# Kernel tuning notes

Measured on AMD Instinct MI355X. Metric: run time of the kernel, lower is better.

## Reference

```python
import jax, jax.numpy as jnp
import numpy as np

N = 131072
MUL = 128                      # multiplicity of each irrep block in the input
IN_DIM = MUL * (1 + 3 + 5)     # 128x0e + 128x1o + 128x2e = 1152
INV_SQRT_MUL = 1.0 / np.sqrt(MUL)  # e3nn o3.Linear path normalization (fan_in = 128)

# --- Clebsch-Gordan (wigner 3j) tensors for 1o x 1o -> 0e, 1e, 2e ------------
# e3nn real basis ordering for l=1 is (y, z, x): index 0=y, 1=z, 2=x.

def _w3j_110():
    # 0e output: dot product; sum of squares of entries = 1
    return np.eye(3, dtype=np.float32) / np.sqrt(3.0)

def _w3j_111():
    # 1e output: Levi-Civita (cross product), normalized so sum of squares = 1
    eps = np.zeros((3, 3, 3), np.float32)
    for i, j, k in [(0, 1, 2), (1, 2, 0), (2, 0, 1)]:
        eps[i, j, k] = 1.0
        eps[j, i, k] = -1.0
    return eps / np.sqrt(6.0)

def _w3j_112():
    # 2e output: symmetric traceless rank-2 part.
    # l=2 component order: (xy, yz, 3z^2-r^2, xz, x^2-y^2); l=1 axes (y,z,x).
    Y, Z, X = 0, 1, 2
    s2 = 1.0 / np.sqrt(2.0)
    s6 = 1.0 / np.sqrt(6.0)
    M = np.zeros((3, 3, 5), np.float32)
    M[X, Y, 0] = M[Y, X, 0] = s2
    M[Y, Z, 1] = M[Z, Y, 1] = s2
    M[X, X, 2] = -s6; M[Y, Y, 2] = -s6; M[Z, Z, 2] = 2.0 * s6
    M[X, Z, 3] = M[Z, X, 3] = s2
    M[X, X, 4] = s2; M[Y, Y, 4] = -s2
    return M / np.sqrt(5.0)

_C0 = jnp.asarray(_w3j_110())
_C1 = jnp.asarray(_w3j_111())
_C2 = jnp.asarray(_w3j_112())
# path weights sqrt(dim(irrep_out)) for irrep_normalization='component',
# path_normalization='element' with fan = mul1*mul2 = 1
_PW0 = 1.0
_PW1 = float(np.sqrt(3.0))
_PW2 = float(np.sqrt(5.0))


def setup_inputs() -> dict:
    key = jax.random.key(0)
    k1, k2, k3, k4 = jax.random.split(key, 4)
    x = jax.random.normal(k1, (N, IN_DIM), jnp.float32)
    W1 = jax.random.normal(k2, (MUL, MUL), jnp.float32)   # 128x1o -> 128x1o
    W2 = jax.random.normal(k3, (MUL, 2), jnp.float32)     # 128x1o -> 2x1o
    tp_w = jax.random.normal(k4, (3,), jnp.float32)       # one weight per CG path
    return {"x": x, "W1": W1, "W2": W2, "tp_w": tp_w}


def reference(x, W1, W2, tp_w):
    n = x.shape[0]
    # o3.Linear(128x0e+128x1o+128x2e -> 128x1o): only the 1o block connects.
    x1o = x[:, MUL:MUL + 3 * MUL].reshape(n, MUL, 3)
    y = jnp.einsum('nuc,uv->nvc', x1o, W1) * INV_SQRT_MUL   # [N,128,3]
    y = jax.nn.silu(y)                                      # elementwise, as in torch
    y = jnp.einsum('nuc,uv->nvc', y, W2) * INV_SQRT_MUL     # [N,2,3] == 2x1o
    a, b = y[:, 0], y[:, 1]                                 # split y[:, :3], y[:, 3:]
    out0 = (tp_w[0] * _PW0) * jnp.einsum('ij,ni,nj->n', _C0, a, b)[:, None]  # [N,1]
    out1 = (tp_w[1] * _PW1) * jnp.einsum('ijk,ni,nj->nk', _C1, a, b)          # [N,3]
    out2 = (tp_w[2] * _PW2) * jnp.einsum('ijk,ni,nj->nk', _C2, a, b)          # [N,5]
    return jnp.concatenate([out0, out1, out2], axis=-1)     # [N,9] (0e+1e+2e)
```

## Files before the change

kernel.cpp:

```cpp
#include <hip/hip_runtime.h>
#include <hip/hip_bf16.h>

#define MULC 128
#define IN_DIM 1152
#define ROWS_PER_WG 64
#define NTHREADS 256

typedef __attribute__((ext_vector_type(8))) short bf16x8;
typedef __attribute__((ext_vector_type(4))) float f32x4;
typedef __attribute__((ext_vector_type(4))) unsigned short u16x4;

#define W1T_PITCH 136
#define A_BASE 17408
#define A_PITCH 40
#define A_PLANE 2560

__device__ __forceinline__ unsigned short f2bf(float f) {
    unsigned int b = __builtin_bit_cast(unsigned int, f);
    b += 0x7fffu + ((b >> 16) & 1u);
    return (unsigned short)(b >> 16);
}

__global__ __launch_bounds__(NTHREADS, 2)
void nltp_kernel(const float* __restrict__ x, const float* __restrict__ W1,
                 const float* __restrict__ W2, const float* __restrict__ tpw,
                 float* __restrict__ out)
{
    __shared__ __align__(16) unsigned short lds[25088];
    const int t  = threadIdx.x;
    const int n0 = blockIdx.x * ROWS_PER_WG;
    const int l  = t & 63;
    const int w  = t >> 6;
    const int g  = l >> 4;
    const int li = l & 15;

    for (int it = 0; it < 16; ++it) {
        int tau = it * 256 + t;
        int v   = tau & 127;
        int u   = (tau >> 7) * 4;
        float f0 = W1[(u + 0) * MULC + v];
        float f1 = W1[(u + 1) * MULC + v];
        float f2 = W1[(u + 2) * MULC + v];
        float f3 = W1[(u + 3) * MULC + v];
        u16x4 pk = { f2bf(f0), f2bf(f1), f2bf(f2), f2bf(f3) };
        *(u16x4*)&lds[v * W1T_PITCH + u] = pk;
    }

    f32x4 acc[3][8];
#pragma unroll
    for (int c = 0; c < 3; ++c)
#pragma unroll
        for (int nt = 0; nt < 8; ++nt)
            acc[c][nt] = (f32x4){0.f, 0.f, 0.f, 0.f};

    for (int kc = 0; kc < 4; ++kc) {
        __syncthreads();
#pragma unroll
        for (int q = 0; q < 2; ++q) {
            int idx = q * 256 + t;
            int r   = idx >> 3;
            int j   = idx & 7;
            const float* src = x + (size_t)(n0 + r) * IN_DIM + MULC + kc * 96 + j * 12;
            float4 v0 = *(const float4*)(src);
            float4 v1 = *(const float4*)(src + 4);
            float4 v2 = *(const float4*)(src + 8);
            u16x4 p0 = { f2bf(v0.x), f2bf(v0.w), f2bf(v1.z), f2bf(v2.y) };
            u16x4 p1 = { f2bf(v0.y), f2bf(v1.x), f2bf(v1.w), f2bf(v2.z) };
            u16x4 p2 = { f2bf(v0.z), f2bf(v1.y), f2bf(v2.x), f2bf(v2.w) };
            int base = A_BASE + r * A_PITCH + 4 * j;
            *(u16x4*)&lds[base]              = p0;
            *(u16x4*)&lds[base + A_PLANE]    = p1;
            *(u16x4*)&lds[base + 2 * A_PLANE] = p2;
        }
        __syncthreads();

        bf16x8 af[3];
#pragma unroll
        for (int c = 0; c < 3; ++c)
            af[c] = *(const bf16x8*)&lds[A_BASE + c * A_PLANE + (16 * w + li) * A_PITCH + g * 8];
#pragma unroll
        for (int nt = 0; nt < 8; ++nt) {
            bf16x8 bf = *(const bf16x8*)&lds[(nt * 16 + li) * W1T_PITCH + kc * 32 + g * 8];
#pragma unroll
            for (int c = 0; c < 3; ++c)
                acc[c][nt] = __builtin_amdgcn_mfma_f32_16x16x32_bf16(af[c], bf, acc[c][nt], 0, 0, 0);
        }
    }

    const float inv = 0.08838834764831845f;
    float w2a[8], w2b[8];
#pragma unroll
    for (int nt = 0; nt < 8; ++nt) {
        float2 p = *(const float2*)(W2 + 2 * (nt * 16 + li));
        w2a[nt] = p.x; w2b[nt] = p.y;
    }
    float pa[3][4], pb[3][4];
#pragma unroll
    for (int c = 0; c < 3; ++c)
#pragma unroll
        for (int rg = 0; rg < 4; ++rg) { pa[c][rg] = 0.f; pb[c][rg] = 0.f; }

#pragma unroll
    for (int c = 0; c < 3; ++c)
#pragma unroll
        for (int nt = 0; nt < 8; ++nt)
#pragma unroll
            for (int rg = 0; rg < 4; ++rg) {
                float y = acc[c][nt][rg] * inv;
                float s = y / (1.f + __expf(-y));
                pa[c][rg] += s * w2a[nt];
                pb[c][rg] += s * w2b[nt];
            }

#pragma unroll
    for (int c = 0; c < 3; ++c)
#pragma unroll
        for (int rg = 0; rg < 4; ++rg) {
            float va = pa[c][rg], vb = pb[c][rg];
            va += __shfl_xor(va, 1, 16); vb += __shfl_xor(vb, 1, 16);
            va += __shfl_xor(va, 2, 16); vb += __shfl_xor(vb, 2, 16);
            va += __shfl_xor(va, 4, 16); vb += __shfl_xor(vb, 4, 16);
            va += __shfl_xor(va, 8, 16); vb += __shfl_xor(vb, 8, 16);
            pa[c][rg] = va * inv;
            pb[c][rg] = vb * inv;
        }

    const float tw0 = tpw[0], tw1 = tpw[1], tw2 = tpw[2];
    const float k0 = tw0 * 0.5773502691896258f;
    const float k1 = tw1 * 0.7071067811865476f;
    const float s2 = 0.7071067811865476f;
    const float s6 = 0.4082482904638631f;

#pragma unroll
    for (int rg = 0; rg < 4; ++rg) {
        float a0 = pa[0][rg], a1 = pa[1][rg], a2 = pa[2][rg];
        float b0 = pb[0][rg], b1 = pb[1][rg], b2 = pb[2][rg];
        float o0 = k0 * (a0 * b0 + a1 * b1 + a2 * b2);
        float o1 = k1 * (a1 * b2 - a2 * b1);
        float o2 = k1 * (a2 * b0 - a0 * b2);
        float o3 = k1 * (a0 * b1 - a1 * b0);
        float o4 = tw2 * (s2 * (a2 * b0 + a0 * b2));
        float o5 = tw2 * (s2 * (a0 * b1 + a1 * b0));
        float o6 = tw2 * (s6 * (2.f * a1 * b1 - a2 * b2 - a0 * b0));
        float o7 = tw2 * (s2 * (a2 * b1 + a1 * b2));
        float o8 = tw2 * (s2 * (a2 * b2 - a0 * b0));
        float o = li == 0 ? o0 : li == 1 ? o1 : li == 2 ? o2 : li == 3 ? o3 :
                  li == 4 ? o4 : li == 5 ? o5 : li == 6 ? o6 : li == 7 ? o7 : o8;
        if (li < 9) {
            int row = n0 + 16 * w + 4 * g + rg;
            out[row * 9 + li] = o;
        }
    }
}

extern "C" void kernel_launch(void* const* d_in, const int* in_sizes, int n_in,
                              void* d_out, int out_size, void* d_ws, size_t ws_size,
                              hipStream_t stream) {
    const float* x   = (const float*)d_in[0];
    const float* W1  = (const float*)d_in[1];
    const float* W2  = (const float*)d_in[2];
    const float* tpw = (const float*)d_in[3];
    float* out = (float*)d_out;
    const int n = in_sizes[0] / IN_DIM;
    dim3 grid(n / ROWS_PER_WG);
    nltp_kernel<<<grid, NTHREADS, 0, stream>>>(x, W1, W2, tpw, out);
}
```

Before: 62.81 us.

## Load x fragments directly into registers with double-buffered prefetch, drop LDS staging

Each lane now loads its own 24 contiguous floats of x per k-chunk straight into registers and converts them to bf16 MFMA A-fragments, instead of staging them through LDS with barriers. Loads for the next chunk are issued before the current chunk's MFMAs, and the first chunk load overlaps the W1 transpose into LDS. This removes per-chunk LDS writes, reads and syncthreads and shrinks LDS use. In exchange it raises register pressure, and the global loads are less coalesced across lanes.

```diff
diff --git a/kernel.cpp b/kernel.cpp
--- a/kernel.cpp
+++ b/kernel.cpp
@@ -5,15 +5,11 @@
 #define IN_DIM 1152
 #define ROWS_PER_WG 64
 #define NTHREADS 256
+#define W1T_PITCH 136
 
 typedef __attribute__((ext_vector_type(8))) short bf16x8;
 typedef __attribute__((ext_vector_type(4))) float f32x4;
 typedef __attribute__((ext_vector_type(4))) unsigned short u16x4;
-
-#define W1T_PITCH 136
-#define A_BASE 17408
-#define A_PITCH 40
-#define A_PLANE 2560
 
 __device__ __forceinline__ unsigned short f2bf(float f) {
     unsigned int b = __builtin_bit_cast(unsigned int, f);
@@ -21,18 +17,47 @@
     return (unsigned short)(b >> 16);
 }
 
+#define LOADC(r0,r1,r2,r3,r4,r5, kc) {                                  \
+    const float4* p_ = (const float4*)(xbase + 96 * (kc));              \
+    r0 = p_[0]; r1 = p_[1]; r2 = p_[2]; r3 = p_[3]; r4 = p_[4]; r5 = p_[5]; }
+
+#define FRAGS(F0,F1,F2, r0,r1,r2,r3,r4,r5)                                         \
+    bf16x8 F0 = { (short)f2bf(r0.x), (short)f2bf(r0.w), (short)f2bf(r1.z),         \
+                  (short)f2bf(r2.y), (short)f2bf(r3.x), (short)f2bf(r3.w),         \
+                  (short)f2bf(r4.z), (short)f2bf(r5.y) };                          \
+    bf16x8 F1 = { (short)f2bf(r0.y), (short)f2bf(r1.x), (short)f2bf(r1.w),         \
+                  (short)f2bf(r2.z), (short)f2bf(r3.y), (short)f2bf(r4.x),         \
+                  (short)f2bf(r4.w), (short)f2bf(r5.z) };                          \
+    bf16x8 F2 = { (short)f2bf(r0.z), (short)f2bf(r1.y), (short)f2bf(r2.x),         \
+                  (short)f2bf(r2.w), (short)f2bf(r3.z), (short)f2bf(r4.y),         \
+                  (short)f2bf(r5.x), (short)f2bf(r5.w) };
+
+#define MFMA_STEP(kc, F0,F1,F2)                                                     \
+    _Pragma("unroll")                                                               \
+    for (int nt = 0; nt < 8; ++nt) {                                                \
+        bf16x8 bfr = *(const bf16x8*)&lds[(nt * 16 + li) * W1T_PITCH + (kc) * 32 + g * 8]; \
+        acc[0][nt] = __builtin_amdgcn_mfma_f32_16x16x32_bf16(F0, bfr, acc[0][nt], 0, 0, 0); \
+        acc[1][nt] = __builtin_amdgcn_mfma_f32_16x16x32_bf16(F1, bfr, acc[1][nt], 0, 0, 0); \
+        acc[2][nt] = __builtin_amdgcn_mfma_f32_16x16x32_bf16(F2, bfr, acc[2][nt], 0, 0, 0); \
+    }
+
 __global__ __launch_bounds__(NTHREADS, 2)
 void nltp_kernel(const float* __restrict__ x, const float* __restrict__ W1,
                  const float* __restrict__ W2, const float* __restrict__ tpw,
                  float* __restrict__ out)
 {
-    __shared__ __align__(16) unsigned short lds[25088];
+    __shared__ __align__(16) unsigned short lds[128 * W1T_PITCH];
     const int t  = threadIdx.x;
     const int n0 = blockIdx.x * ROWS_PER_WG;
     const int l  = t & 63;
     const int w  = t >> 6;
     const int g  = l >> 4;
     const int li = l & 15;
+
+    const float* xbase = x + (size_t)(n0 + 16 * w + li) * IN_DIM + MULC + 24 * g;
+
+    float4 a0,a1,a2,a3,a4,a5, b0,b1,b2,b3,b4,b5;
+    LOADC(a0,a1,a2,a3,a4,a5, 0);
 
     for (int it = 0; it < 16; ++it) {
         int tau = it * 256 + t;
@@ -45,6 +70,7 @@
         u16x4 pk = { f2bf(f0), f2bf(f1), f2bf(f2), f2bf(f3) };
         *(u16x4*)&lds[v * W1T_PITCH + u] = pk;
     }
+    __syncthreads();
 
     f32x4 acc[3][8];
 #pragma unroll
@@ -53,39 +79,13 @@
         for (int nt = 0; nt < 8; ++nt)
             acc[c][nt] = (f32x4){0.f, 0.f, 0.f, 0.f};
 
-    for (int kc = 0; kc < 4; ++kc) {
-        __syncthreads();
-#pragma unroll
-        for (int q = 0; q < 2; ++q) {
-            int idx = q * 256 + t;
-            int r   = idx >> 3;
-            int j   = idx & 7;
-            const float* src = x + (size_t)(n0 + r) * IN_DIM + MULC + kc * 96 + j * 12;
-            float4 v0 = *(const float4*)(src);
-            float4 v1 = *(const float4*)(src + 4);
-            float4 v2 = *(const float4*)(src + 8);
-            u16x4 p0 = { f2bf(v0.x), f2bf(v0.w), f2bf(v1.z), f2bf(v2.y) };
-            u16x4 p1 = { f2bf(v0.y), f2bf(v1.x), f2bf(v1.w), f2bf(v2.z) };
-            u16x4 p2 = { f2bf(v0.z), f2bf(v1.y), f2bf(v2.x), f2bf(v2.w) };
-            int base = A_BASE + r * A_PITCH + 4 * j;
-            *(u16x4*)&lds[base]              = p0;
-            *(u16x4*)&lds[base + A_PLANE]    = p1;
-            *(u16x4*)&lds[base + 2 * A_PLANE] = p2;
-        }
-        __syncthreads();
-
-        bf16x8 af[3];
-#pragma unroll
-        for (int c = 0; c < 3; ++c)
-            af[c] = *(const bf16x8*)&lds[A_BASE + c * A_PLANE + (16 * w + li) * A_PITCH + g * 8];
-#pragma unroll
-        for (int nt = 0; nt < 8; ++nt) {
-            bf16x8 bf = *(const bf16x8*)&lds[(nt * 16 + li) * W1T_PITCH + kc * 32 + g * 8];
-#pragma unroll
-            for (int c = 0; c < 3; ++c)
-                acc[c][nt] = __builtin_amdgcn_mfma_f32_16x16x32_bf16(af[c], bf, acc[c][nt], 0, 0, 0);
-        }
-    }
+    LOADC(b0,b1,b2,b3,b4,b5, 1);
+    { FRAGS(fa0,fa1,fa2, a0,a1,a2,a3,a4,a5); MFMA_STEP(0, fa0,fa1,fa2); }
+    LOADC(a0,a1,a2,a3,a4,a5, 2);
+    { FRAGS(fb0,fb1,fb2, b0,b1,b2,b3,b4,b5); MFMA_STEP(1, fb0,fb1,fb2); }
+    LOADC(b0,b1,b2,b3,b4,b5, 3);
+    { FRAGS(fc0,fc1,fc2, a0,a1,a2,a3,a4,a5); MFMA_STEP(2, fc0,fc1,fc2); }
+    { FRAGS(fd0,fd1,fd2, b0,b1,b2,b3,b4,b5); MFMA_STEP(3, fd0,fd1,fd2); }
 
     const float inv = 0.08838834764831845f;
     float w2a[8], w2b[8];
@@ -133,17 +133,17 @@
 
 #pragma unroll
     for (int rg = 0; rg < 4; ++rg) {
-        float a0 = pa[0][rg], a1 = pa[1][rg], a2 = pa[2][rg];
-        float b0 = pb[0][rg], b1 = pb[1][rg], b2 = pb[2][rg];
-        float o0 = k0 * (a0 * b0 + a1 * b1 + a2 * b2);
-        float o1 = k1 * (a1 * b2 - a2 * b1);
-        float o2 = k1 * (a2 * b0 - a0 * b2);
-        float o3 = k1 * (a0 * b1 - a1 * b0);
-        float o4 = tw2 * (s2 * (a2 * b0 + a0 * b2));
-        float o5 = tw2 * (s2 * (a0 * b1 + a1 * b0));
-        float o6 = tw2 * (s6 * (2.f * a1 * b1 - a2 * b2 - a0 * b0));
-        float o7 = tw2 * (s2 * (a2 * b1 + a1 * b2));
-        float o8 = tw2 * (s2 * (a2 * b2 - a0 * b0));
+        float a_0 = pa[0][rg], a_1 = pa[1][rg], a_2 = pa[2][rg];
+        float b_0 = pb[0][rg], b_1 = pb[1][rg], b_2 = pb[2][rg];
+        float o0 = k0 * (a_0 * b_0 + a_1 * b_1 + a_2 * b_2);
+        float o1 = k1 * (a_1 * b_2 - a_2 * b_1);
+        float o2 = k1 * (a_2 * b_0 - a_0 * b_2);
+        float o3 = k1 * (a_0 * b_1 - a_1 * b_0);
+        float o4 = tw2 * (s2 * (a_2 * b_0 + a_0 * b_2));
+        float o5 = tw2 * (s2 * (a_0 * b_1 + a_1 * b_0));
+        float o6 = tw2 * (s6 * (2.f * a_1 * b_1 - a_2 * b_2 - a_0 * b_0));
+        float o7 = tw2 * (s2 * (a_2 * b_1 + a_1 * b_2));
+        float o8 = tw2 * (s2 * (a_2 * b_2 - a_0 * b_0));
         float o = li == 0 ? o0 : li == 1 ? o1 : li == 2 ? o2 : li == 3 ? o3 :
                   li == 4 ? o4 : li == 5 ? o5 : li == 6 ? o6 : li == 7 ? o7 : o8;
         if (li < 9) {
```

Result: slower. 64.73 us (+3.1%).
